# Kernel optimization log

Hardware: AMD Instinct MI355X
Metric: run time of the kernel (lower is better)

The kernel has to match this reference:

```python
import jax, jax.numpy as jnp
import numpy as np

N, B, E = 50000, 1, 800000
D_IN = 128      # input_size == out_size (residual)
HID = 128       # hidden_size
H = 4           # heads
C = HID // H    # per-head dim = 32
EPS = 1e-5


def setup_inputs() -> dict:
    key = jax.random.key(0)
    ks = jax.random.split(key, 16)
    s_in = 1.0 / np.sqrt(D_IN)
    s_hid = 1.0 / np.sqrt(HID)
    return {
        "x": jax.random.normal(ks[0], (N, B, D_IN), jnp.float32),
        "edge_index": jax.random.randint(ks[1], (2, E), 0, N, jnp.int64 if jax.config.jax_enable_x64 else jnp.int32),
        "edge_attr": jax.random.normal(ks[2], (E, HID), jnp.float32),
        # TransformerConv projections (weights stored torch-style [out, in])
        "Wq": jax.random.uniform(ks[3], (HID, D_IN), jnp.float32, -s_in, s_in),
        "bq": jnp.zeros((HID,), jnp.float32),
        "Wk": jax.random.uniform(ks[4], (HID, D_IN), jnp.float32, -s_in, s_in),
        "bk": jnp.zeros((HID,), jnp.float32),
        "Wv": jax.random.uniform(ks[5], (HID, D_IN), jnp.float32, -s_in, s_in),
        "bv": jnp.zeros((HID,), jnp.float32),
        "We": jax.random.uniform(ks[6], (HID, HID), jnp.float32, -s_hid, s_hid),  # lin_edge, no bias
        "Wskip": jax.random.uniform(ks[7], (HID, D_IN), jnp.float32, -s_in, s_in),
        "bskip": jnp.zeros((HID,), jnp.float32),
        "Wp": jax.random.uniform(ks[8], (HID, HID), jnp.float32, -s_hid, s_hid),   # physics_linear
        "bp": jnp.zeros((HID,), jnp.float32),
        "Wm": jax.random.uniform(ks[9], (D_IN, HID), jnp.float32, -s_hid, s_hid),  # merge_linear
        "bm": jnp.zeros((D_IN,), jnp.float32),
    }


def reference(x, edge_index, edge_attr, Wq, bq, Wk, bk, Wv, bv, We,
              Wskip, bskip, Wp, bp, Wm, bm):
    n = x.shape[0]
    src, dst = edge_index[0], edge_index[1]  # message flows src -> dst (j -> i)

    # node-wise QKV projections -> [N, B, H, C]
    q = (x @ Wq.T + bq).reshape(n, B, H, C)
    k = (x @ Wk.T + bk).reshape(n, B, H, C)
    v = (x @ Wv.T + bv).reshape(n, B, H, C)

    # edge feature projection -> [E, H, C]
    e = (edge_attr @ We.T).reshape(-1, H, C)

    # per-edge attention scores [E, B, H]
    k_j = k[src] + e[:, None]                       # [E, B, H, C]
    alpha = (q[dst] * k_j).sum(-1) / jnp.sqrt(jnp.asarray(C, x.dtype))

    # scatter-softmax over incoming edges of each dst node
    m = jax.ops.segment_max(alpha, dst, num_segments=n)      # [N, B, H]
    a = jnp.exp(alpha - m[dst])
    s = jax.ops.segment_sum(a, dst, num_segments=n)
    alpha = a / s[dst]

    # weighted scatter-add aggregation
    msg = (v[src] + e[:, None]) * alpha[..., None]           # [E, B, H, C]
    out = jax.ops.segment_sum(msg, dst, num_segments=n)      # [N, B, H, C]
    out = out.reshape(n, B, H * C)

    # root skip connection
    out = out + (x @ Wskip.T + bskip)

    # GraphResidualBlock tail
    out = jax.nn.relu(out)
    out = out @ Wp.T + bp
    # custom LayerNorm: normalize over the node dim (dim 0), weight/bias unused
    mu = out.mean(0, keepdims=True)
    sd = out.std(0, keepdims=True)
    out = (out - mu) / (sd + EPS)
    out = jax.nn.relu(out)
    out = out @ Wm.T + bm
    return out + x
```

## Files before the change

kernel.cpp:

```cpp
#include <hip/hip_runtime.h>
#include <stdint.h>

#define RS32 0.17677669529663687f

typedef short bf16x8 __attribute__((ext_vector_type(8)));
typedef float f32x4 __attribute__((ext_vector_type(4)));

__device__ __forceinline__ ushort f2bf(float f) {
  uint32_t b = __float_as_uint(f);
  b = (b + 0x7fffu + ((b >> 16) & 1u)) >> 16;
  return (ushort)b;
}
__device__ __forceinline__ float bflo(uint32_t w) { return __uint_as_float(w << 16); }
__device__ __forceinline__ float bfhi(uint32_t w) { return __uint_as_float(w & 0xffff0000u); }
__device__ __forceinline__ float bfu(ushort s) { return __uint_as_float(((uint32_t)s) << 16); }

__launch_bounds__(256)
__global__ void proj_direct_kernel(const ushort* __restrict__ xb16,
                                   const ushort* __restrict__ Wb,
                                   const ushort* __restrict__ Mtb,
                                   const float* __restrict__ bk, const float* __restrict__ bv,
                                   const float* __restrict__ bs, const float* __restrict__ bq,
                                   const float* __restrict__ bu,
                                   ushort* __restrict__ skipb, ushort* __restrict__ kvi,
                                   ushort* __restrict__ u, ushort* __restrict__ qb, int N)
{
  const int y = blockIdx.y;
  const ushort* Wsrc = (y < 4) ? (Wb + (size_t)y * 16384) : (Mtb + (size_t)(y - 4) * 16384);

  const int tid = threadIdx.x;
  const int nb = blockIdx.x * 128;
  const int lane = tid & 63, wv = tid >> 6;
  const int wr = (wv >> 1) * 64, wc = (wv & 1) * 64;
  const int fr = lane & 15, fq = lane >> 4;

  f32x4 acc[4][4];
#pragma unroll
  for (int m = 0; m < 4; ++m)
#pragma unroll
    for (int n = 0; n < 4; ++n) acc[m][n] = (f32x4)0.0f;

#pragma unroll
  for (int kk = 0; kk < 4; ++kk) {
    const int ko = kk * 32 + fq * 8;
    bf16x8 af[4], bf[4];
#pragma unroll
    for (int m = 0; m < 4; ++m)
      af[m] = *(const bf16x8*)(xb16 + (size_t)(nb + wr + m * 16 + fr) * 128 + ko);
#pragma unroll
    for (int n = 0; n < 4; ++n)
      bf[n] = *(const bf16x8*)(Wsrc + (size_t)(wc + n * 16 + fr) * 128 + ko);
#pragma unroll
    for (int m = 0; m < 4; ++m)
#pragma unroll
      for (int n = 0; n < 4; ++n)
        acc[m][n] = __builtin_amdgcn_mfma_f32_16x16x32_bf16(af[m], bf[n], acc[m][n], 0, 0, 0);
  }

  float bcol[4];
#pragma unroll
  for (int n = 0; n < 4; ++n) {
    const int c = wc + n * 16 + fr;
    bcol[n] = (y == 0) ? bk[c] : (y == 1) ? bv[c] : (y == 2) ? bs[c]
            : (y == 3) ? bq[c] : bu[(y - 4) * 128 + c];
  }
#pragma unroll
  for (int m = 0; m < 4; ++m) {
    const int r0 = nb + wr + m * 16 + fq * 4;
#pragma unroll
    for (int r = 0; r < 4; ++r) {
      const int gr = r0 + r;
      if (gr < N) {
#pragma unroll
        for (int n = 0; n < 4; ++n) {
          const int c = wc + n * 16 + fr;
          float o = acc[m][n][r] + bcol[n];
          if (y == 2)      skipb[(size_t)gr * 128 + c] = f2bf(o);
          else if (y == 3) qb[(size_t)gr * 128 + c] = f2bf(o);
          else if (y == 0) kvi[(size_t)gr * 256 + (c >> 2) * 8 + (c & 3)] = f2bf(o);
          else if (y == 1) kvi[(size_t)gr * 256 + (c >> 2) * 8 + 4 + (c & 3)] = f2bf(o);
          else             u[(size_t)gr * 512 + (y - 4) * 128 + c] = f2bf(o);
        }
      }
    }
  }
}

__global__ void x2bf_kernel(const float* __restrict__ x, ushort* __restrict__ xb, int total4)
{
  int i = blockIdx.x * 256 + threadIdx.x;
  if (i < total4) {
    float4 v = ((const float4*)x)[i];
    uint2 w = make_uint2((uint32_t)f2bf(v.x) | ((uint32_t)f2bf(v.y) << 16),
                         (uint32_t)f2bf(v.z) | ((uint32_t)f2bf(v.w) << 16));
    ((uint2*)xb)[i] = w;
  }
}

__global__ void prep_wb_kernel(const float* __restrict__ Wk, const float* __restrict__ Wv,
                               const float* __restrict__ Ws, const float* __restrict__ Wq,
                               ushort* __restrict__ Wb)
{
  int i = blockIdx.x * 256 + threadIdx.x;
  if (i >= 4 * 16384) return;
  int y = i >> 14, r = i & 16383;
  const float* src = (y == 0) ? Wk : (y == 1) ? Wv : (y == 2) ? Ws : Wq;
  Wb[i] = f2bf(src[r]);
}

__global__ void prep_w2_kernel(const float* __restrict__ Wp, const float* __restrict__ Wm,
                               ushort* __restrict__ Wpb, ushort* __restrict__ Wmb)
{
  int i = blockIdx.x * 256 + threadIdx.x;
  if (i < 16384) { Wpb[i] = f2bf(Wp[i]); Wmb[i] = f2bf(Wm[i]); }
}

__global__ void prep_mt_kernel(const float* __restrict__ Wq, const float* __restrict__ We,
                               ushort* __restrict__ Mtb)
{
  const int tid = threadIdx.x;
  const int jp = blockIdx.x * 2 + (tid >> 7);
  const int d = tid & 127;
  const int h = jp >> 7, j = jp & 127;
  const float* wq = Wq + (size_t)(32 * h) * 128 + d;
  const float* we = We + (size_t)(32 * h) * 128 + j;
  float acc = 0.f;
#pragma unroll 8
  for (int a = 0; a < 32; ++a) acc = fmaf(wq[a * 128], we[a * 128], acc);
  Mtb[(size_t)jp * 128 + d] = f2bf(acc);
}

__global__ void prep_bu_kernel(const float* __restrict__ bq, const float* __restrict__ We,
                               float* __restrict__ bu)
{
  const int jp = threadIdx.x;
  const int h = jp >> 7, j = jp & 127;
  float acc = 0.f;
  for (int a = 0; a < 32; ++a)
    acc = fmaf(bq[32 * h + a], We[(size_t)(32 * h + a) * 128 + j], acc);
  bu[jp] = acc;
}

__global__ void prep_web_kernel(const float* __restrict__ We, ushort* __restrict__ WeB)
{
  int idx = blockIdx.x * 256 + threadIdx.x;
  if (idx >= 128 * 512) return;
  int c = idx >> 9, j = idx & 511;
  int hh = j >> 7, k2 = j & 127;
  WeB[idx] = (hh == (c >> 5)) ? f2bf(We[(size_t)c * 128 + k2]) : (ushort)0;
}

__global__ void deg_kernel(const int* __restrict__ ei, int* __restrict__ deg, int E)
{
  int e = blockIdx.x * 256 + threadIdx.x;
  if (e < E) atomicAdd(&deg[ei[E + e]], 1);
}

__launch_bounds__(256)
__global__ void start_kernel(const int* __restrict__ deg, int* __restrict__ offs,
                             int* __restrict__ cursor, int* __restrict__ gcount, int N)
{
  const int i = blockIdx.x * 256 + threadIdx.x;
  const int lane = threadIdx.x & 63;
  int d = (i < N) ? deg[i] : 0;
  int scan = d;
#pragma unroll
  for (int ofs = 1; ofs < 64; ofs <<= 1) {
    int t = __shfl_up(scan, ofs, 64);
    if (lane >= ofs) scan += t;
  }
  int total = __shfl(scan, 63, 64);
  int base = 0;
  if (lane == 63) base = atomicAdd(gcount, total);
  base = __shfl(base, 63, 64);
  int excl = base + scan - d;
  if (i < N) { offs[i] = excl; cursor[i] = excl; }
}

__global__ void fill_kernel(const int* __restrict__ ei, int* __restrict__ cursor,
                            int2* __restrict__ csr, int E)
{
  int e = blockIdx.x * 256 + threadIdx.x;
  if (e < E) {
    int dst = ei[E + e];
    int slot = atomicAdd(&cursor[dst], 1);
    csr[slot] = make_int2(ei[e], e);
  }
}

__launch_bounds__(256)
__global__ void fused_attn2_kernel(const int2* __restrict__ csr, const int* __restrict__ offs,
                                   const int* __restrict__ deg,
                                   const ushort* __restrict__ qb, const ushort* __restrict__ kvi,
                                   const ushort* __restrict__ u,
                                   const float* __restrict__ eattr,
                                   ushort* __restrict__ aggS, float* __restrict__ wsS, int N)
{
  const int tid = threadIdx.x;
  const int lane = tid & 63;
  const int wid = tid >> 6;
  const int p = lane >> 5;
  const int j32 = lane & 31;
  const int c0 = j32 * 4;
  const int h = j32 >> 3;
  const int gwave = blockIdx.x * 4 + wid;
  const int nwaves = gridDim.x * 4;

  for (int n = gwave; n < N; n += nwaves) {
    const int e0 = offs[n];
    const int e1 = e0 + deg[n];

    const uint2 qp = *(const uint2*)(qb + (size_t)n * 128 + c0);
    uint2 uhp[4];
#pragma unroll
    for (int hh = 0; hh < 4; ++hh)
      uhp[hh] = *(const uint2*)(u + (size_t)n * 512 + hh * 128 + c0);

    float ws0 = 0.f, ws1 = 0.f, ws2 = 0.f, ws3 = 0.f;
    float ax[4][4];
#pragma unroll
    for (int hh = 0; hh < 4; ++hh)
#pragma unroll
      for (int j = 0; j < 4; ++j) ax[hh][j] = 0.f;
    float sm0 = 0.f, sm1 = 0.f, sm2 = 0.f, sm3 = 0.f;

    int sl = e0 + p;
    if (sl < e1) {
      int2 seC = csr[sl];
      float4 eaC = *(const float4*)(eattr + (size_t)seC.y * 128 + c0);
      uint4 kvC = *(const uint4*)(kvi + (size_t)seC.x * 256 + j32 * 8);
      int sln = sl + 2;
      int2 seN = (sln < e1) ? csr[sln] : seC;
      for (; sl < e1; sl += 2) {
        float4 eaN = *(const float4*)(eattr + (size_t)seN.y * 128 + c0);
        uint4 kvN = *(const uint4*)(kvi + (size_t)seN.x * 256 + j32 * 8);
        const int slf = sl + 4;
        int2 seF = (slf < e1) ? csr[slf] : seN;

        float P0 = eaC.x * bflo(uhp[0].x) + eaC.y * bfhi(uhp[0].x)
                 + eaC.z * bflo(uhp[0].y) + eaC.w * bfhi(uhp[0].y);
        float P1 = eaC.x * bflo(uhp[1].x) + eaC.y * bfhi(uhp[1].x)
                 + eaC.z * bflo(uhp[1].y) + eaC.w * bfhi(uhp[1].y);
        float P2 = eaC.x * bflo(uhp[2].x) + eaC.y * bfhi(uhp[2].x)
                 + eaC.z * bflo(uhp[2].y) + eaC.w * bfhi(uhp[2].y);
        float P3 = eaC.x * bflo(uhp[3].x) + eaC.y * bfhi(uhp[3].x)
                 + eaC.z * bflo(uhp[3].y) + eaC.w * bfhi(uhp[3].y);
        const float qk = bflo(qp.x) * bflo(kvC.x) + bfhi(qp.x) * bfhi(kvC.x)
                       + bflo(qp.y) * bflo(kvC.y) + bfhi(qp.y) * bfhi(kvC.y);
        P0 += (h == 0) ? qk : 0.f;
        P1 += (h == 1) ? qk : 0.f;
        P2 += (h == 2) ? qk : 0.f;
        P3 += (h == 3) ? qk : 0.f;
#pragma unroll
        for (int mm = 1; mm <= 16; mm <<= 1) {
          P0 += __shfl_xor(P0, mm, 64);
          P1 += __shfl_xor(P1, mm, 64);
          P2 += __shfl_xor(P2, mm, 64);
          P3 += __shfl_xor(P3, mm, 64);
        }
        const float a0 = __expf(P0 * RS32);
        const float a1 = __expf(P1 * RS32);
        const float a2 = __expf(P2 * RS32);
        const float a3 = __expf(P3 * RS32);
        sm0 += a0; sm1 += a1; sm2 += a2; sm3 += a3;
        const float aV = (h == 0) ? a0 : (h == 1) ? a1 : (h == 2) ? a2 : a3;
        ws0 = fmaf(aV, bflo(kvC.z), ws0); ws1 = fmaf(aV, bfhi(kvC.z), ws1);
        ws2 = fmaf(aV, bflo(kvC.w), ws2); ws3 = fmaf(aV, bfhi(kvC.w), ws3);
        ax[0][0] = fmaf(a0, eaC.x, ax[0][0]); ax[0][1] = fmaf(a0, eaC.y, ax[0][1]);
        ax[0][2] = fmaf(a0, eaC.z, ax[0][2]); ax[0][3] = fmaf(a0, eaC.w, ax[0][3]);
        ax[1][0] = fmaf(a1, eaC.x, ax[1][0]); ax[1][1] = fmaf(a1, eaC.y, ax[1][1]);
        ax[1][2] = fmaf(a1, eaC.z, ax[1][2]); ax[1][3] = fmaf(a1, eaC.w, ax[1][3]);
        ax[2][0] = fmaf(a2, eaC.x, ax[2][0]); ax[2][1] = fmaf(a2, eaC.y, ax[2][1]);
        ax[2][2] = fmaf(a2, eaC.z, ax[2][2]); ax[2][3] = fmaf(a2, eaC.w, ax[2][3]);
        ax[3][0] = fmaf(a3, eaC.x, ax[3][0]); ax[3][1] = fmaf(a3, eaC.y, ax[3][1]);
        ax[3][2] = fmaf(a3, eaC.z, ax[3][2]); ax[3][3] = fmaf(a3, eaC.w, ax[3][3]);

        eaC = eaN; kvC = kvN; seN = seF;
      }
    }

#pragma unroll
    for (int hh = 0; hh < 4; ++hh)
#pragma unroll
      for (int j = 0; j < 4; ++j) ax[hh][j] += __shfl_xor(ax[hh][j], 32, 64);
    ws0 += __shfl_xor(ws0, 32, 64); ws1 += __shfl_xor(ws1, 32, 64);
    ws2 += __shfl_xor(ws2, 32, 64); ws3 += __shfl_xor(ws3, 32, 64);
    sm0 += __shfl_xor(sm0, 32, 64); sm1 += __shfl_xor(sm1, 32, 64);
    sm2 += __shfl_xor(sm2, 32, 64); sm3 += __shfl_xor(sm3, 32, 64);

    const float iv0 = (sm0 > 0.f) ? 1.f / sm0 : 0.f;
    const float iv1 = (sm1 > 0.f) ? 1.f / sm1 : 0.f;
    const float iv2 = (sm2 > 0.f) ? 1.f / sm2 : 0.f;
    const float iv3 = (sm3 > 0.f) ? 1.f / sm3 : 0.f;

    if (p == 0) {
      const float s = (h == 0) ? iv0 : (h == 1) ? iv1 : (h == 2) ? iv2 : iv3;
      *(float4*)(wsS + (size_t)n * 128 + c0) =
          make_float4(ws0 * s, ws1 * s, ws2 * s, ws3 * s);
    }

    float o0[4], o1[4], s0, s1;
    if (p == 0) {
#pragma unroll
      for (int j = 0; j < 4; ++j) { o0[j] = ax[0][j]; o1[j] = ax[1][j]; }
      s0 = iv0; s1 = iv1;
    } else {
#pragma unroll
      for (int j = 0; j < 4; ++j) { o0[j] = ax[2][j]; o1[j] = ax[3][j]; }
      s0 = iv2; s1 = iv3;
    }
    uint2 w0 = make_uint2(((uint32_t)f2bf(o0[0] * s0)) | (((uint32_t)f2bf(o0[1] * s0)) << 16),
                          ((uint32_t)f2bf(o0[2] * s0)) | (((uint32_t)f2bf(o0[3] * s0)) << 16));
    uint2 w1 = make_uint2(((uint32_t)f2bf(o1[0] * s1)) | (((uint32_t)f2bf(o1[1] * s1)) << 16),
                          ((uint32_t)f2bf(o1[2] * s1)) | (((uint32_t)f2bf(o1[3] * s1)) << 16));
    *(uint2*)(aggS + (size_t)n * 512 + (p * 2) * 128 + c0) = w0;
    *(uint2*)(aggS + (size_t)n * 512 + (p * 2 + 1) * 128 + c0) = w1;
  }
}

__launch_bounds__(256)
__global__ void fused_post_kernel(const ushort* __restrict__ aggS, const ushort* __restrict__ WeB,
                                  const float* __restrict__ wsS, const ushort* __restrict__ skipb,
                                  const ushort* __restrict__ Wpb, const float* __restrict__ bp,
                                  float* __restrict__ t1,
                                  float* __restrict__ sums, float* __restrict__ sumsq, int N)
{
  __shared__ ushort smem[2 * 128 * 72];
  ushort* As = smem;
  ushort* Bs = smem + 128 * 72;
  const int tid = threadIdx.x;
  const int nb = blockIdx.x * 128;
  const int lane = tid & 63, wv = tid >> 6;
  const int wr = (wv >> 1) * 64, wc = (wv & 1) * 64;
  const int fr = lane & 15, fq = lane >> 4;
  const int r = tid >> 1, cs = (tid & 1) * 32;

  f32x4 acc[4][4];
#pragma unroll
  for (int m = 0; m < 4; ++m)
#pragma unroll
    for (int n = 0; n < 4; ++n) acc[m][n] = (f32x4)0.0f;

  for (int kc = 0; kc < 512; kc += 64) {
    uint4 av[4], bv[4];
    if (nb + r < N) {
      const uint4* src = (const uint4*)(aggS + (size_t)(nb + r) * 512 + kc + cs);
      av[0] = src[0]; av[1] = src[1]; av[2] = src[2]; av[3] = src[3];
    } else {
#pragma unroll
      for (int i = 0; i < 4; ++i) av[i] = make_uint4(0, 0, 0, 0);
    }
    {
      const uint4* src = (const uint4*)(WeB + (size_t)r * 512 + kc + cs);
      bv[0] = src[0]; bv[1] = src[1]; bv[2] = src[2]; bv[3] = src[3];
    }
    if (kc) __syncthreads();
#pragma unroll
    for (int i = 0; i < 4; ++i) {
      *(uint4*)&As[r * 72 + cs + i * 8] = av[i];
      *(uint4*)&Bs[r * 72 + cs + i * 8] = bv[i];
    }
    __syncthreads();

#pragma unroll
    for (int s = 0; s < 2; ++s) {
      bf16x8 ah[4], bh[4];
#pragma unroll
      for (int m = 0; m < 4; ++m)
        ah[m] = *(const bf16x8*)&As[(wr + m * 16 + fr) * 72 + s * 32 + fq * 8];
#pragma unroll
      for (int n = 0; n < 4; ++n)
        bh[n] = *(const bf16x8*)&Bs[(wc + n * 16 + fr) * 72 + s * 32 + fq * 8];
#pragma unroll
      for (int m = 0; m < 4; ++m)
#pragma unroll
        for (int n = 0; n < 4; ++n)
          acc[m][n] = __builtin_amdgcn_mfma_f32_16x16x32_bf16(ah[m], bh[n], acc[m][n], 0, 0, 0);
    }
  }
  __syncthreads();

  ushort* zs = smem;
#pragma unroll
  for (int m = 0; m < 4; ++m) {
    const int lr0 = wr + m * 16 + fq * 4;
#pragma unroll
    for (int rr = 0; rr < 4; ++rr) {
      const int lrow = lr0 + rr;
      const int gr = nb + lrow;
#pragma unroll
      for (int n = 0; n < 4; ++n) {
        const int c = wc + n * 16 + fr;
        float o = 0.f;
        if (gr < N) {
          o = acc[m][n][rr] + wsS[(size_t)gr * 128 + c] + bfu(skipb[(size_t)gr * 128 + c]);
          o = fmaxf(o, 0.f);
        }
        zs[lrow * 136 + c] = f2bf(o);
      }
    }
  }
  __syncthreads();

  f32x4 acc2[4][4];
#pragma unroll
  for (int m = 0; m < 4; ++m)
#pragma unroll
    for (int n = 0; n < 4; ++n) acc2[m][n] = (f32x4)0.0f;
#pragma unroll
  for (int kk = 0; kk < 4; ++kk) {
    const int ko = kk * 32 + fq * 8;
    bf16x8 af[4], bf[4];
#pragma unroll
    for (int m = 0; m < 4; ++m)
      af[m] = *(const bf16x8*)&zs[(wr + m * 16 + fr) * 136 + ko];
#pragma unroll
    for (int n = 0; n < 4; ++n)
      bf[n] = *(const bf16x8*)(Wpb + (size_t)(wc + n * 16 + fr) * 128 + ko);
#pragma unroll
    for (int m = 0; m < 4; ++m)
#pragma unroll
      for (int n = 0; n < 4; ++n)
        acc2[m][n] = __builtin_amdgcn_mfma_f32_16x16x32_bf16(af[m], bf[n], acc2[m][n], 0, 0, 0);
  }

  float bcol[4];
#pragma unroll
  for (int n = 0; n < 4; ++n) bcol[n] = bp[wc + n * 16 + fr];
  float csum[4] = {0.f, 0.f, 0.f, 0.f}, csum2[4] = {0.f, 0.f, 0.f, 0.f};
#pragma unroll
  for (int m = 0; m < 4; ++m) {
    const int r0 = nb + wr + m * 16 + fq * 4;
#pragma unroll
    for (int rr = 0; rr < 4; ++rr) {
      const int gr = r0 + rr;
      if (gr < N) {
#pragma unroll
        for (int n = 0; n < 4; ++n) {
          const int c = wc + n * 16 + fr;
          float o = acc2[m][n][rr] + bcol[n];
          t1[(size_t)gr * 128 + c] = o;
          csum[n] += o; csum2[n] = fmaf(o, o, csum2[n]);
        }
      }
    }
  }
#pragma unroll
  for (int n = 0; n < 4; ++n) {
    csum[n] += __shfl_xor(csum[n], 16, 64);
    csum[n] += __shfl_xor(csum[n], 32, 64);
    csum2[n] += __shfl_xor(csum2[n], 16, 64);
    csum2[n] += __shfl_xor(csum2[n], 32, 64);
  }
  if (fq == 0) {
#pragma unroll
    for (int n = 0; n < 4; ++n) {
      atomicAdd(&sums[wc + n * 16 + fr], csum[n]);
      atomicAdd(&sumsq[wc + n * 16 + fr], csum2[n]);
    }
  }
}

__global__ void finalize_stats_kernel(const float* __restrict__ sums, const float* __restrict__ sumsq,
                                      float* __restrict__ mu, float* __restrict__ inv, int N)
{
  int c = threadIdx.x;
  float m = sums[c] / (float)N;
  float var = sumsq[c] / (float)N - m * m;
  float sd = sqrtf(fmaxf(var, 0.f));
  mu[c] = m;
  inv[c] = 1.f / (sd + 1e-5f);
}

__global__ void z2_kernel(const float* __restrict__ t1, const float* __restrict__ mu,
                          const float* __restrict__ inv, ushort* __restrict__ zb, int total4)
{
  int i = blockIdx.x * 256 + threadIdx.x;
  if (i < total4) {
    const int c0 = (i & 31) * 4;
    float4 v = ((const float4*)t1)[i];
    float4 m4 = *(const float4*)(mu + c0);
    float4 i4 = *(const float4*)(inv + c0);
    float z0 = fmaxf((v.x - m4.x) * i4.x, 0.f);
    float z1 = fmaxf((v.y - m4.y) * i4.y, 0.f);
    float z2v = fmaxf((v.z - m4.z) * i4.z, 0.f);
    float z3 = fmaxf((v.w - m4.w) * i4.w, 0.f);
    uint2 w = make_uint2((uint32_t)f2bf(z0) | ((uint32_t)f2bf(z1) << 16),
                         (uint32_t)f2bf(z2v) | ((uint32_t)f2bf(z3) << 16));
    ((uint2*)zb)[i] = w;
  }
}

__launch_bounds__(256)
__global__ void out_gemm_kernel(const ushort* __restrict__ zb, const ushort* __restrict__ Wmb,
                                const float* __restrict__ bm, const float* __restrict__ x,
                                float* __restrict__ out, int N)
{
  const int tid = threadIdx.x;
  const int nb = blockIdx.x * 128;
  const int lane = tid & 63, wv = tid >> 6;
  const int wr = (wv >> 1) * 64, wc = (wv & 1) * 64;
  const int fr = lane & 15, fq = lane >> 4;

  f32x4 acc[4][4];
#pragma unroll
  for (int m = 0; m < 4; ++m)
#pragma unroll
    for (int n = 0; n < 4; ++n) acc[m][n] = (f32x4)0.0f;

#pragma unroll
  for (int kk = 0; kk < 4; ++kk) {
    const int ko = kk * 32 + fq * 8;
    bf16x8 af[4], bf[4];
#pragma unroll
    for (int m = 0; m < 4; ++m)
      af[m] = *(const bf16x8*)(zb + (size_t)(nb + wr + m * 16 + fr) * 128 + ko);
#pragma unroll
    for (int n = 0; n < 4; ++n)
      bf[n] = *(const bf16x8*)(Wmb + (size_t)(wc + n * 16 + fr) * 128 + ko);
#pragma unroll
    for (int m = 0; m < 4; ++m)
#pragma unroll
      for (int n = 0; n < 4; ++n)
        acc[m][n] = __builtin_amdgcn_mfma_f32_16x16x32_bf16(af[m], bf[n], acc[m][n], 0, 0, 0);
  }

  float bcol[4];
#pragma unroll
  for (int n = 0; n < 4; ++n) bcol[n] = bm[wc + n * 16 + fr];
#pragma unroll
  for (int m = 0; m < 4; ++m) {
    const int r0 = nb + wr + m * 16 + fq * 4;
#pragma unroll
    for (int r = 0; r < 4; ++r) {
      const int gr = r0 + r;
      if (gr < N) {
#pragma unroll
        for (int n = 0; n < 4; ++n) {
          const int c = wc + n * 16 + fr;
          out[(size_t)gr * 128 + c] = acc[m][n][r] + bcol[n] + x[(size_t)gr * 128 + c];
        }
      }
    }
  }
}

extern "C" void kernel_launch(void* const* d_in, const int* in_sizes, int n_in,
                              void* d_out, int out_size, void* d_ws, size_t ws_size,
                              hipStream_t stream) {
  const float* x    = (const float*)d_in[0];
  const int*   ei   = (const int*)d_in[1];
  const float* eatt = (const float*)d_in[2];
  const float* Wq = (const float*)d_in[3];  const float* bq = (const float*)d_in[4];
  const float* Wk = (const float*)d_in[5];  const float* bk = (const float*)d_in[6];
  const float* Wv = (const float*)d_in[7];  const float* bv = (const float*)d_in[8];
  const float* We = (const float*)d_in[9];
  const float* Wsk = (const float*)d_in[10]; const float* bsk = (const float*)d_in[11];
  const float* Wp = (const float*)d_in[12]; const float* bp = (const float*)d_in[13];
  const float* Wm = (const float*)d_in[14]; const float* bm = (const float*)d_in[15];
  float* out = (float*)d_out;

  const int N = in_sizes[0] / 128;
  const int E = in_sizes[1] / 2;

  char* w = (char*)d_ws;
  auto alloc = [&](size_t bytes) {
    char* p = w;
    w += (bytes + 255) & ~(size_t)255;
    return p;
  };
  const size_t node_f = (size_t)N * 128 * sizeof(float);
  float*  wsA  = (float*)alloc(node_f);
  float*  t1   = (float*)alloc(node_f);
  ushort* xb16 = (ushort*)alloc((size_t)N * 128 * sizeof(ushort));
  ushort* skipb= (ushort*)alloc((size_t)N * 128 * sizeof(ushort));
  ushort* qb   = (ushort*)alloc((size_t)N * 128 * sizeof(ushort));
  ushort* zb   = (ushort*)alloc((size_t)N * 128 * sizeof(ushort));
  ushort* kvi  = (ushort*)alloc((size_t)N * 256 * sizeof(ushort));
  ushort* u    = (ushort*)alloc((size_t)N * 512 * sizeof(ushort));
  ushort* aggS = (ushort*)alloc((size_t)N * 512 * sizeof(ushort));
  ushort* WeB  = (ushort*)alloc(128 * 512 * sizeof(ushort));
  ushort* Wb   = (ushort*)alloc(4 * 128 * 128 * sizeof(ushort));
  ushort* Mtb  = (ushort*)alloc(512 * 128 * sizeof(ushort));
  ushort* Wpb  = (ushort*)alloc(128 * 128 * sizeof(ushort));
  ushort* Wmb  = (ushort*)alloc(128 * 128 * sizeof(ushort));
  float*  bu   = (float*)alloc(512 * sizeof(float));
  int*    deg  = (int*)alloc((size_t)N * sizeof(int));
  int*    offs = (int*)alloc((size_t)N * sizeof(int));
  int*    curs = (int*)alloc((size_t)N * sizeof(int));
  int*    gcnt = (int*)alloc(sizeof(int));
  int2*   csr  = (int2*)alloc((size_t)E * sizeof(int2));
  float*  sums  = (float*)alloc(128 * sizeof(float));
  float*  sumsq = (float*)alloc(128 * sizeof(float));
  float*  mu    = (float*)alloc(128 * sizeof(float));
  float*  inv   = (float*)alloc(128 * sizeof(float));
  (void)ws_size; (void)n_in; (void)out_size;

  const int NB = (N + 127) / 128;
  const int EB = (E + 255) / 256;

  hipMemsetAsync(deg, 0, (size_t)N * sizeof(int), stream);
  hipMemsetAsync(gcnt, 0, sizeof(int), stream);
  hipMemsetAsync(sums, 0, 2 * 128 * sizeof(float), stream);

  x2bf_kernel<<<(N * 32 + 255) / 256, 256, 0, stream>>>(x, xb16, N * 32);
  prep_wb_kernel<<<256, 256, 0, stream>>>(Wk, Wv, Wsk, Wq, Wb);
  prep_w2_kernel<<<64, 256, 0, stream>>>(Wp, Wm, Wpb, Wmb);
  prep_mt_kernel<<<256, 256, 0, stream>>>(Wq, We, Mtb);
  prep_bu_kernel<<<1, 512, 0, stream>>>(bq, We, bu);
  prep_web_kernel<<<256, 256, 0, stream>>>(We, WeB);

  proj_direct_kernel<<<dim3(NB, 8), 256, 0, stream>>>(xb16, Wb, Mtb, bk, bv, bsk, bq, bu,
                                                      skipb, kvi, u, qb, N);

  deg_kernel<<<EB, 256, 0, stream>>>(ei, deg, E);
  start_kernel<<<(N + 255) / 256, 256, 0, stream>>>(deg, offs, curs, gcnt, N);
  fill_kernel<<<EB, 256, 0, stream>>>(ei, curs, csr, E);

  fused_attn2_kernel<<<2048, 256, 0, stream>>>(csr, offs, deg, qb, kvi, u, eatt,
                                               aggS, wsA, N);

  fused_post_kernel<<<NB, 256, 0, stream>>>(aggS, WeB, wsA, skipb, Wpb, bp,
                                            t1, sums, sumsq, N);
  finalize_stats_kernel<<<1, 128, 0, stream>>>(sums, sumsq, mu, inv, N);

  z2_kernel<<<(N * 32 + 255) / 256, 256, 0, stream>>>(t1, mu, inv, zb, N * 32);
  out_gemm_kernel<<<NB, 256, 0, stream>>>(zb, Wmb, bm, x, out, N);
}
```

Before: 479.4 us.

## Merge prep kernels, fuse normalization into output GEMM, store ws in bf16

Five weight-prep kernels become one launch, and three memsets become one by placing deg, gcnt and the stat sums in a contiguous zeroed region. The z2 normalize/ReLU/bf16 pass is folded into the A-operand load of the output GEMM, which removes one full N×128 write and read. The per-node weighted-sum buffer passed from attention to the post kernel is now stored as bf16 instead of fp32, halving that traffic at some precision cost. The fused GEMM now reads fp32 t1, twice the bytes of the old bf16 zb, and recomputes the normalization per tile.

```diff
diff --git a/kernel.cpp b/kernel.cpp
--- a/kernel.cpp
+++ b/kernel.cpp
@@ -97,57 +97,50 @@
   }
 }
 
-__global__ void prep_wb_kernel(const float* __restrict__ Wk, const float* __restrict__ Wv,
-                               const float* __restrict__ Ws, const float* __restrict__ Wq,
-                               ushort* __restrict__ Wb)
+__global__ void prep_all_kernel(const float* __restrict__ Wk, const float* __restrict__ Wv,
+                                const float* __restrict__ Ws, const float* __restrict__ Wq,
+                                const float* __restrict__ Wp, const float* __restrict__ Wm,
+                                const float* __restrict__ We, const float* __restrict__ bq,
+                                ushort* __restrict__ Wb, ushort* __restrict__ Wpb,
+                                ushort* __restrict__ Wmb, ushort* __restrict__ WeB,
+                                ushort* __restrict__ Mtb, float* __restrict__ bu)
 {
   int i = blockIdx.x * 256 + threadIdx.x;
-  if (i >= 4 * 16384) return;
-  int y = i >> 14, r = i & 16383;
-  const float* src = (y == 0) ? Wk : (y == 1) ? Wv : (y == 2) ? Ws : Wq;
-  Wb[i] = f2bf(src[r]);
-}
-
-__global__ void prep_w2_kernel(const float* __restrict__ Wp, const float* __restrict__ Wm,
-                               ushort* __restrict__ Wpb, ushort* __restrict__ Wmb)
-{
-  int i = blockIdx.x * 256 + threadIdx.x;
-  if (i < 16384) { Wpb[i] = f2bf(Wp[i]); Wmb[i] = f2bf(Wm[i]); }
-}
-
-__global__ void prep_mt_kernel(const float* __restrict__ Wq, const float* __restrict__ We,
-                               ushort* __restrict__ Mtb)
-{
-  const int tid = threadIdx.x;
-  const int jp = blockIdx.x * 2 + (tid >> 7);
-  const int d = tid & 127;
-  const int h = jp >> 7, j = jp & 127;
-  const float* wq = Wq + (size_t)(32 * h) * 128 + d;
-  const float* we = We + (size_t)(32 * h) * 128 + j;
-  float acc = 0.f;
+  if (i < 65536) {
+    int y = i >> 14, r = i & 16383;
+    const float* src = (y == 0) ? Wk : (y == 1) ? Wv : (y == 2) ? Ws : Wq;
+    Wb[i] = f2bf(src[r]);
+    return;
+  }
+  i -= 65536;
+  if (i < 16384) { Wpb[i] = f2bf(Wp[i]); Wmb[i] = f2bf(Wm[i]); return; }
+  i -= 16384;
+  if (i < 65536) {
+    int c = i >> 9, j = i & 511;
+    int hh = j >> 7, k2 = j & 127;
+    WeB[i] = (hh == (c >> 5)) ? f2bf(We[(size_t)c * 128 + k2]) : (ushort)0;
+    return;
+  }
+  i -= 65536;
+  if (i < 65536) {
+    int jp = i >> 7, d = i & 127;
+    int h = jp >> 7, j = jp & 127;
+    const float* wq = Wq + (size_t)(32 * h) * 128 + d;
+    const float* we = We + (size_t)(32 * h) * 128 + j;
+    float acc = 0.f;
 #pragma unroll 8
-  for (int a = 0; a < 32; ++a) acc = fmaf(wq[a * 128], we[a * 128], acc);
-  Mtb[(size_t)jp * 128 + d] = f2bf(acc);
-}
-
-__global__ void prep_bu_kernel(const float* __restrict__ bq, const float* __restrict__ We,
-                               float* __restrict__ bu)
-{
-  const int jp = threadIdx.x;
-  const int h = jp >> 7, j = jp & 127;
-  float acc = 0.f;
-  for (int a = 0; a < 32; ++a)
-    acc = fmaf(bq[32 * h + a], We[(size_t)(32 * h + a) * 128 + j], acc);
-  bu[jp] = acc;
-}
-
-__global__ void prep_web_kernel(const float* __restrict__ We, ushort* __restrict__ WeB)
-{
-  int idx = blockIdx.x * 256 + threadIdx.x;
-  if (idx >= 128 * 512) return;
-  int c = idx >> 9, j = idx & 511;
-  int hh = j >> 7, k2 = j & 127;
-  WeB[idx] = (hh == (c >> 5)) ? f2bf(We[(size_t)c * 128 + k2]) : (ushort)0;
+    for (int a = 0; a < 32; ++a) acc = fmaf(wq[a * 128], we[a * 128], acc);
+    Mtb[i] = f2bf(acc);
+    return;
+  }
+  i -= 65536;
+  if (i < 512) {
+    int h = i >> 7, j = i & 127;
+    float acc = 0.f;
+    for (int a = 0; a < 32; ++a)
+      acc = fmaf(bq[32 * h + a], We[(size_t)(32 * h + a) * 128 + j], acc);
+    bu[i] = acc;
+  }
 }
 
 __global__ void deg_kernel(const int* __restrict__ ei, int* __restrict__ deg, int E)
@@ -194,7 +187,7 @@
                                    const ushort* __restrict__ qb, const ushort* __restrict__ kvi,
                                    const ushort* __restrict__ u,
                                    const float* __restrict__ eattr,
-                                   ushort* __restrict__ aggS, float* __restrict__ wsS, int N)
+                                   ushort* __restrict__ aggS, ushort* __restrict__ wsb, int N)
 {
   const int tid = threadIdx.x;
   const int lane = tid & 63;
@@ -295,8 +288,9 @@
 
     if (p == 0) {
       const float s = (h == 0) ? iv0 : (h == 1) ? iv1 : (h == 2) ? iv2 : iv3;
-      *(float4*)(wsS + (size_t)n * 128 + c0) =
-          make_float4(ws0 * s, ws1 * s, ws2 * s, ws3 * s);
+      uint2 w = make_uint2(((uint32_t)f2bf(ws0 * s)) | (((uint32_t)f2bf(ws1 * s)) << 16),
+                           ((uint32_t)f2bf(ws2 * s)) | (((uint32_t)f2bf(ws3 * s)) << 16));
+      *(uint2*)(wsb + (size_t)n * 128 + c0) = w;
     }
 
     float o0[4], o1[4], s0, s1;
@@ -320,7 +314,7 @@
 
 __launch_bounds__(256)
 __global__ void fused_post_kernel(const ushort* __restrict__ aggS, const ushort* __restrict__ WeB,
-                                  const float* __restrict__ wsS, const ushort* __restrict__ skipb,
+                                  const ushort* __restrict__ wsb, const ushort* __restrict__ skipb,
                                   const ushort* __restrict__ Wpb, const float* __restrict__ bp,
                                   float* __restrict__ t1,
                                   float* __restrict__ sums, float* __restrict__ sumsq, int N)
@@ -393,7 +387,7 @@
         const int c = wc + n * 16 + fr;
         float o = 0.f;
         if (gr < N) {
-          o = acc[m][n][rr] + wsS[(size_t)gr * 128 + c] + bfu(skipb[(size_t)gr * 128 + c]);
+          o = acc[m][n][rr] + bfu(wsb[(size_t)gr * 128 + c]) + bfu(skipb[(size_t)gr * 128 + c]);
           o = fmaxf(o, 0.f);
         }
         zs[lrow * 136 + c] = f2bf(o);
@@ -472,27 +466,10 @@
   inv[c] = 1.f / (sd + 1e-5f);
 }
 
-__global__ void z2_kernel(const float* __restrict__ t1, const float* __restrict__ mu,
-                          const float* __restrict__ inv, ushort* __restrict__ zb, int total4)
-{
-  int i = blockIdx.x * 256 + threadIdx.x;
-  if (i < total4) {
-    const int c0 = (i & 31) * 4;
-    float4 v = ((const float4*)t1)[i];
-    float4 m4 = *(const float4*)(mu + c0);
-    float4 i4 = *(const float4*)(inv + c0);
-    float z0 = fmaxf((v.x - m4.x) * i4.x, 0.f);
-    float z1 = fmaxf((v.y - m4.y) * i4.y, 0.f);
-    float z2v = fmaxf((v.z - m4.z) * i4.z, 0.f);
-    float z3 = fmaxf((v.w - m4.w) * i4.w, 0.f);
-    uint2 w = make_uint2((uint32_t)f2bf(z0) | ((uint32_t)f2bf(z1) << 16),
-                         (uint32_t)f2bf(z2v) | ((uint32_t)f2bf(z3) << 16));
-    ((uint2*)zb)[i] = w;
-  }
-}
-
 __launch_bounds__(256)
-__global__ void out_gemm_kernel(const ushort* __restrict__ zb, const ushort* __restrict__ Wmb,
+__global__ void out_gemm_kernel(const float* __restrict__ t1, const float* __restrict__ mu,
+                                const float* __restrict__ inv,
+                                const ushort* __restrict__ Wmb,
                                 const float* __restrict__ bm, const float* __restrict__ x,
                                 float* __restrict__ out, int N)
 {
@@ -511,10 +488,29 @@
 #pragma unroll
   for (int kk = 0; kk < 4; ++kk) {
     const int ko = kk * 32 + fq * 8;
+    const float4 m0 = *(const float4*)(mu + ko);
+    const float4 m1 = *(const float4*)(mu + ko + 4);
+    const float4 i0 = *(const float4*)(inv + ko);
+    const float4 i1 = *(const float4*)(inv + ko + 4);
     bf16x8 af[4], bf[4];
 #pragma unroll
-    for (int m = 0; m < 4; ++m)
-      af[m] = *(const bf16x8*)(zb + (size_t)(nb + wr + m * 16 + fr) * 128 + ko);
+    for (int m = 0; m < 4; ++m) {
+      const int gr = nb + wr + m * 16 + fr;
+      float4 v0 = make_float4(0.f, 0.f, 0.f, 0.f), v1 = v0;
+      if (gr < N) {
+        v0 = *(const float4*)(t1 + (size_t)gr * 128 + ko);
+        v1 = *(const float4*)(t1 + (size_t)gr * 128 + ko + 4);
+      }
+      float z[8];
+      z[0] = fmaxf((v0.x - m0.x) * i0.x, 0.f); z[1] = fmaxf((v0.y - m0.y) * i0.y, 0.f);
+      z[2] = fmaxf((v0.z - m0.z) * i0.z, 0.f); z[3] = fmaxf((v0.w - m0.w) * i0.w, 0.f);
+      z[4] = fmaxf((v1.x - m1.x) * i1.x, 0.f); z[5] = fmaxf((v1.y - m1.y) * i1.y, 0.f);
+      z[6] = fmaxf((v1.z - m1.z) * i1.z, 0.f); z[7] = fmaxf((v1.w - m1.w) * i1.w, 0.f);
+      bf16x8 a;
+#pragma unroll
+      for (int j = 0; j < 8; ++j) a[j] = (short)f2bf(z[j]);
+      af[m] = a;
+    }
 #pragma unroll
     for (int n = 0; n < 4; ++n)
       bf[n] = *(const bf16x8*)(Wmb + (size_t)(wc + n * 16 + fr) * 128 + ko);
@@ -570,12 +566,11 @@
     return p;
   };
   const size_t node_f = (size_t)N * 128 * sizeof(float);
-  float*  wsA  = (float*)alloc(node_f);
   float*  t1   = (float*)alloc(node_f);
   ushort* xb16 = (ushort*)alloc((size_t)N * 128 * sizeof(ushort));
   ushort* skipb= (ushort*)alloc((size_t)N * 128 * sizeof(ushort));
   ushort* qb   = (ushort*)alloc((size_t)N * 128 * sizeof(ushort));
-  ushort* zb   = (ushort*)alloc((size_t)N * 128 * sizeof(ushort));
+  ushort* wsb  = (ushort*)alloc((size_t)N * 128 * sizeof(ushort));
   ushort* kvi  = (ushort*)alloc((size_t)N * 256 * sizeof(ushort));
   ushort* u    = (ushort*)alloc((size_t)N * 512 * sizeof(ushort));
   ushort* aggS = (ushort*)alloc((size_t)N * 512 * sizeof(ushort));
@@ -585,30 +580,26 @@
   ushort* Wpb  = (ushort*)alloc(128 * 128 * sizeof(ushort));
   ushort* Wmb  = (ushort*)alloc(128 * 128 * sizeof(ushort));
   float*  bu   = (float*)alloc(512 * sizeof(float));
-  int*    deg  = (int*)alloc((size_t)N * sizeof(int));
   int*    offs = (int*)alloc((size_t)N * sizeof(int));
   int*    curs = (int*)alloc((size_t)N * sizeof(int));
-  int*    gcnt = (int*)alloc(sizeof(int));
   int2*   csr  = (int2*)alloc((size_t)E * sizeof(int2));
-  float*  sums  = (float*)alloc(128 * sizeof(float));
-  float*  sumsq = (float*)alloc(128 * sizeof(float));
   float*  mu    = (float*)alloc(128 * sizeof(float));
   float*  inv   = (float*)alloc(128 * sizeof(float));
+  char*   zp   = alloc((size_t)N * 4 + 1536);
+  int*    deg  = (int*)zp;
+  int*    gcnt = (int*)(zp + (size_t)N * 4);
+  float*  sums = (float*)(zp + (size_t)N * 4 + 256);
+  float*  sumsq= sums + 128;
   (void)ws_size; (void)n_in; (void)out_size;
 
   const int NB = (N + 127) / 128;
   const int EB = (E + 255) / 256;
 
-  hipMemsetAsync(deg, 0, (size_t)N * sizeof(int), stream);
-  hipMemsetAsync(gcnt, 0, sizeof(int), stream);
-  hipMemsetAsync(sums, 0, 2 * 128 * sizeof(float), stream);
+  hipMemsetAsync(zp, 0, (size_t)N * 4 + 1536, stream);
 
   x2bf_kernel<<<(N * 32 + 255) / 256, 256, 0, stream>>>(x, xb16, N * 32);
-  prep_wb_kernel<<<256, 256, 0, stream>>>(Wk, Wv, Wsk, Wq, Wb);
-  prep_w2_kernel<<<64, 256, 0, stream>>>(Wp, Wm, Wpb, Wmb);
-  prep_mt_kernel<<<256, 256, 0, stream>>>(Wq, We, Mtb);
-  prep_bu_kernel<<<1, 512, 0, stream>>>(bq, We, bu);
-  prep_web_kernel<<<256, 256, 0, stream>>>(We, WeB);
+  prep_all_kernel<<<(213504 + 255) / 256, 256, 0, stream>>>(Wk, Wv, Wsk, Wq, Wp, Wm, We, bq,
+                                                            Wb, Wpb, Wmb, WeB, Mtb, bu);
 
   proj_direct_kernel<<<dim3(NB, 8), 256, 0, stream>>>(xb16, Wb, Mtb, bk, bv, bsk, bq, bu,
                                                       skipb, kvi, u, qb, N);
@@ -618,12 +609,11 @@
   fill_kernel<<<EB, 256, 0, stream>>>(ei, curs, csr, E);
 
   fused_attn2_kernel<<<2048, 256, 0, stream>>>(csr, offs, deg, qb, kvi, u, eatt,
-                                               aggS, wsA, N);
-
-  fused_post_kernel<<<NB, 256, 0, stream>>>(aggS, WeB, wsA, skipb, Wpb, bp,
+                                               aggS, wsb, N);
+
+  fused_post_kernel<<<NB, 256, 0, stream>>>(aggS, WeB, wsb, skipb, Wpb, bp,
                                             t1, sums, sumsq, N);
   finalize_stats_kernel<<<1, 128, 0, stream>>>(sums, sumsq, mu, inv, N);
 
-  z2_kernel<<<(N * 32 + 255) / 256, 256, 0, stream>>>(t1, mu, inv, zb, N * 32);
-  out_gemm_kernel<<<NB, 256, 0, stream>>>(zb, Wmb, bm, x, out, N);
-}
+  out_gemm_kernel<<<NB, 256, 0, stream>>>(t1, mu, inv, Wmb, bm, x, out, N);
+}
```

Result: faster. 462.0 us (median of 2 runs) (-3.6%).
